# Performance work log

Hardware: AMD Instinct MI355X
Metric: run time of the kernel (lower is better)

## Reference

```python
import jax, jax.numpy as jnp
import numpy as np

N_NODES = 100000
N_EDGES = 1600000
HID = 128


def setup_inputs() -> dict:
    key = jax.random.key(0)
    ks = jax.random.split(key, 9)
    return {
        "x": jax.random.normal(ks[0], (N_NODES, 3), dtype=jnp.float32),
        "edge_index": jax.random.randint(ks[1], (2, N_EDGES), 0, N_NODES, dtype=jnp.int64),
        "W_lift": jax.random.normal(ks[2], (3, HID), dtype=jnp.float32) * 0.1,
        "b_lift": jax.random.normal(ks[3], (HID,), dtype=jnp.float32) * 0.1,
        "W_rel": jax.random.normal(ks[4], (HID, HID), dtype=jnp.float32) * 0.05,
        "b_rel": jax.random.normal(ks[5], (HID,), dtype=jnp.float32) * 0.05,
        "W_root": jax.random.normal(ks[6], (HID, HID), dtype=jnp.float32) * 0.05,
        "W_proj": jax.random.normal(ks[7], (HID, 1), dtype=jnp.float32) * 0.1,
        "b_proj": jax.random.normal(ks[8], (1,), dtype=jnp.float32) * 0.1,
    }


def reference(x, edge_index, W_lift, b_lift, W_rel, b_rel, W_root, W_proj, b_proj):
    # Lifting: [N, 3] -> [N, 128]
    h = x @ W_lift + b_lift
    # GraphConv (PyG): out_i = lin_rel(sum_{j in N(i)} h_j) + lin_root(h_i)
    src, dst = edge_index[0], edge_index[1]
    # gather neighbor features then scatter-add to targets
    agg = jax.ops.segment_sum(h[src], dst, num_segments=N_NODES)  # [N, 128]
    h = agg @ W_rel + b_rel + h @ W_root
    h = jnp.tanh(h)
    # Projection: [N, 128] -> [N, 1]
    return h @ W_proj + b_proj
```

## Files before the change

kernel.cpp:

```cpp
#include <hip/hip_runtime.h>
#include <stdint.h>

#define NN 100000
#define NE 1600000
#define HID 128

#define PSCALE 512.0f
#define PINV   (1.0f / 512.0f)
#define PBIAS  8.0f
#define FMASK  0x7FFFFULL

#define NBINS 391
#define NSLC  8
#define GCAP  768
#define NB3   391
#define TB3   512
#define EB    4096

__device__ __forceinline__ unsigned xcc_id() {
    unsigned x;
    asm volatile("s_getreg_b32 %0, hwreg(HW_REG_XCC_ID)" : "=s"(x));
    return x & (NSLC - 1);
}

__device__ __forceinline__ void prep_weights(
    const float* __restrict__ W_lift, const float* __restrict__ b_lift,
    const float* __restrict__ W_rel, const float* __restrict__ b_rel,
    const float* __restrict__ W_root, float* __restrict__ Wf) {
    int t = threadIdx.x;
    if (t >= HID) return;
    float lr0 = 0.f, lr1 = 0.f, lr2 = 0.f;
    float xr0 = 0.f, xr1 = 0.f, xr2 = 0.f;
    float blr = 0.f, bxr = 0.f;
    for (int k = 0; k < HID; ++k) {
        float wr = W_rel[k * HID + t];
        float wo = W_root[k * HID + t];
        float bl = b_lift[k];
        float a0 = W_lift[0 * HID + k];
        float a1 = W_lift[1 * HID + k];
        float a2 = W_lift[2 * HID + k];
        lr0 += a0 * wr; lr1 += a1 * wr; lr2 += a2 * wr;
        xr0 += a0 * wo; xr1 += a1 * wo; xr2 += a2 * wo;
        blr += bl * wr; bxr += bl * wo;
    }
    Wf[0 * HID + t] = lr0;
    Wf[1 * HID + t] = lr1;
    Wf[2 * HID + t] = lr2;
    Wf[3 * HID + t] = xr0;
    Wf[4 * HID + t] = xr1;
    Wf[5 * HID + t] = xr2;
    Wf[6 * HID + t] = blr;
    Wf[7 * HID + t] = b_rel[t] + bxr;
}

__global__ __launch_bounds__(TB3) void radix4_scatter_prep(
    const int* __restrict__ edges,
    unsigned* __restrict__ galloc,
    unsigned* __restrict__ records,
    const float* __restrict__ W_lift,
    const float* __restrict__ b_lift,
    const float* __restrict__ W_rel,
    const float* __restrict__ b_rel,
    const float* __restrict__ W_root,
    float* __restrict__ Wf) {
    if (blockIdx.x == NB3) {
        prep_weights(W_lift, b_lift, W_rel, b_rel, W_root, Wf);
        return;
    }
    __shared__ unsigned hist[NBINS];
    __shared__ unsigned base[NBINS];
    for (int j = threadIdx.x; j < NBINS; j += TB3) hist[j] = 0;
    __syncthreads();

    const unsigned myxcd = xcc_id();
    const int e0 = blockIdx.x * EB;
    int sreg[8], dreg[8];

#pragma unroll
    for (int k = 0; k < 2; ++k) {
        int eA = e0 + (k * TB3 + threadIdx.x) * 4;
        int4 sv, dv;
        if (eA + 3 < NE) {
            sv = *(const int4*)&edges[eA];
            dv = *(const int4*)&edges[NE + eA];
        } else {
            sv.x = (eA + 0 < NE) ? edges[eA + 0] : -1;
            sv.y = (eA + 1 < NE) ? edges[eA + 1] : -1;
            sv.z = (eA + 2 < NE) ? edges[eA + 2] : -1;
            sv.w = (eA + 3 < NE) ? edges[eA + 3] : -1;
            dv.x = (eA + 0 < NE) ? edges[NE + eA + 0] : -1;
            dv.y = (eA + 1 < NE) ? edges[NE + eA + 1] : -1;
            dv.z = (eA + 2 < NE) ? edges[NE + eA + 2] : -1;
            dv.w = (eA + 3 < NE) ? edges[NE + eA + 3] : -1;
        }
        int ss[4] = { sv.x, sv.y, sv.z, sv.w };
        int dd[4] = { dv.x, dv.y, dv.z, dv.w };
#pragma unroll
        for (int j = 0; j < 4; ++j) {
            bool ok = ((unsigned)ss[j] < NN) && ((unsigned)dd[j] < NN);
            sreg[k * 4 + j] = ok ? ss[j] : -1;
            dreg[k * 4 + j] = ok ? dd[j] : -1;
            if (ok) atomicAdd(&hist[dd[j] >> 8], 1u);
        }
    }
    __syncthreads();
    for (int j = threadIdx.x; j < NBINS; j += TB3) {
        unsigned c = hist[j];
        base[j] = c ? atomicAdd(&galloc[myxcd * NBINS + j], c) : 0u;
        hist[j] = 0;
    }
    __syncthreads();
#pragma unroll
    for (int i = 0; i < 8; ++i) {
        int d = dreg[i];
        if (d < 0) continue;
        int b = d >> 8;
        unsigned pos = base[b] + atomicAdd(&hist[b], 1u);
        if (pos < GCAP)
            records[((size_t)myxcd * NBINS + b) * GCAP + pos] =
                ((unsigned)sreg[i] << 8) | (unsigned)(d & 255);
    }
}

__global__ __launch_bounds__(256) void accum4_node_kernel(
    const unsigned* __restrict__ galloc,
    const unsigned* __restrict__ records,
    const float* __restrict__ x,
    const float* __restrict__ Wf,
    const float* __restrict__ W_proj,
    const float* __restrict__ b_proj,
    float* __restrict__ out) {
    __shared__ unsigned long long acc[256];
    __shared__ float sWt[HID][8];
    __shared__ float sP[HID];
    const int tid = threadIdx.x;
    const int b = blockIdx.x;

    acc[tid] = 0ULL;
    for (int j = tid; j < 8 * HID; j += 256) {
        int r = j >> 7;
        int t = j & (HID - 1);
        sWt[t][r] = Wf[j];
    }
    for (int j = tid; j < HID; j += 256) sP[j] = W_proj[j];
    __syncthreads();

#pragma unroll
    for (int sl = 0; sl < NSLC; ++sl) {
        unsigned cnt = galloc[sl * NBINS + b];
        if (cnt > GCAP) cnt = GCAP;
        const unsigned* rec = records + ((size_t)sl * NBINS + b) * GCAP;
        for (unsigned i = tid; i < cnt; i += 256) {
            unsigned r = rec[i];
            unsigned src = r >> 8;
            const float* xp = x + 3 * (size_t)src;
            unsigned long long u0 = min((unsigned)__float2int_rn((xp[0] + PBIAS) * PSCALE), 8191u);
            unsigned long long u1 = min((unsigned)__float2int_rn((xp[1] + PBIAS) * PSCALE), 8191u);
            unsigned long long u2 = min((unsigned)__float2int_rn((xp[2] + PBIAS) * PSCALE), 8191u);
            atomicAdd(&acc[r & 255u],
                      u0 | (u1 << 19) | (u2 << 38) | (1ULL << 57));
        }
    }
    __syncthreads();

    int node = b * 256 + tid;
    if (node >= NN) return;

    unsigned long long p = acc[tid];
    float degf = (float)(unsigned)(p >> 57);
    float a0 = (float)(unsigned)(p & FMASK) * PINV - PBIAS * degf;
    float a1 = (float)(unsigned)((p >> 19) & FMASK) * PINV - PBIAS * degf;
    float a2 = (float)(unsigned)((p >> 38) & FMASK) * PINV - PBIAS * degf;

    float x0 = x[3 * node + 0];
    float x1 = x[3 * node + 1];
    float x2 = x[3 * node + 2];

    float s = 0.f;
#pragma unroll 8
    for (int t = 0; t < HID; ++t) {
        float4 A = *(const float4*)&sWt[t][0];
        float4 B = *(const float4*)&sWt[t][4];
        float h = B.w
                + a0 * A.x + a1 * A.y + a2 * A.z
                + x0 * A.w + x1 * B.x + x2 * B.y
                + degf * B.z;
        float th = 1.f - 2.f / (__expf(2.f * h) + 1.f);
        s += th * sP[t];
    }
    out[node] = s + b_proj[0];
}

__global__ __launch_bounds__(256) void scatter_prep_kernel(
    const int* __restrict__ edges,
    const float* __restrict__ x,
    unsigned long long* __restrict__ aggp,
    const float* __restrict__ W_lift,
    const float* __restrict__ b_lift,
    const float* __restrict__ W_rel,
    const float* __restrict__ b_rel,
    const float* __restrict__ W_root,
    float* __restrict__ Wf) {
    if (blockIdx.x == 0) {
        prep_weights(W_lift, b_lift, W_rel, b_rel, W_root, Wf);
        return;
    }
    int e = (blockIdx.x - 1) * blockDim.x + threadIdx.x;
    if (e >= NE) return;
    int s = edges[e];
    int d = edges[NE + e];
    if ((unsigned)s >= NN || (unsigned)d >= NN) return;
    float x0 = x[3 * s + 0];
    float x1 = x[3 * s + 1];
    float x2 = x[3 * s + 2];
    unsigned long long u0 = (unsigned)__float2int_rn((x0 + PBIAS) * PSCALE);
    unsigned long long u1 = (unsigned)__float2int_rn((x1 + PBIAS) * PSCALE);
    unsigned long long u2 = (unsigned)__float2int_rn((x2 + PBIAS) * PSCALE);
    atomicAdd(&aggp[d], u0 | (u1 << 19) | (u2 << 38) | (1ULL << 57));
}

__global__ __launch_bounds__(256) void node_kernel(
    const float* __restrict__ x,
    const unsigned long long* __restrict__ aggp,
    const float* __restrict__ Wf,
    const float* __restrict__ W_proj,
    const float* __restrict__ b_proj,
    float* __restrict__ out) {
    __shared__ float sWt[HID][8];
    __shared__ float sP[HID];
    for (int j = threadIdx.x; j < 8 * HID; j += blockDim.x) {
        int r = j >> 7;
        int t = j & (HID - 1);
        sWt[t][r] = Wf[j];
    }
    for (int j = threadIdx.x; j < HID; j += blockDim.x) sP[j] = W_proj[j];
    __syncthreads();

    int i = blockIdx.x * blockDim.x + threadIdx.x;
    if (i >= NN) return;

    unsigned long long p = aggp[i];
    float degf = (float)(unsigned)(p >> 57);
    float a0 = (float)(unsigned)(p & FMASK) * PINV - PBIAS * degf;
    float a1 = (float)(unsigned)((p >> 19) & FMASK) * PINV - PBIAS * degf;
    float a2 = (float)(unsigned)((p >> 38) & FMASK) * PINV - PBIAS * degf;

    float x0 = x[3 * i + 0];
    float x1 = x[3 * i + 1];
    float x2 = x[3 * i + 2];

    float acc = 0.f;
#pragma unroll 8
    for (int t = 0; t < HID; ++t) {
        float4 A = *(const float4*)&sWt[t][0];
        float4 B = *(const float4*)&sWt[t][4];
        float h = B.w
                + a0 * A.x + a1 * A.y + a2 * A.z
                + x0 * A.w + x1 * B.x + x2 * B.y
                + degf * B.z;
        float th = 1.f - 2.f / (__expf(2.f * h) + 1.f);
        acc += th * sP[t];
    }
    out[i] = acc + b_proj[0];
}

extern "C" void kernel_launch(void* const* d_in, const int* in_sizes, int n_in,
                              void* d_out, int out_size, void* d_ws, size_t ws_size,
                              hipStream_t stream) {
    const float* x      = (const float*)d_in[0];
    const int*   edges  = (const int*)d_in[1];
    const float* W_lift = (const float*)d_in[2];
    const float* b_lift = (const float*)d_in[3];
    const float* W_rel  = (const float*)d_in[4];
    const float* b_rel  = (const float*)d_in[5];
    const float* W_root = (const float*)d_in[6];
    const float* W_proj = (const float*)d_in[7];
    const float* b_proj = (const float*)d_in[8];
    float* out = (float*)d_out;

    const size_t off_rec = 1 << 16;
    const size_t off_wf  = off_rec + (size_t)NSLC * NBINS * GCAP * 4;
    const size_t needed  = off_wf + 8 * HID * sizeof(float);

    if (ws_size >= needed) {
        unsigned* galloc = (unsigned*)d_ws;
        unsigned* records = (unsigned*)((char*)d_ws + off_rec);
        float* Wf = (float*)((char*)d_ws + off_wf);

        hipMemsetAsync(galloc, 0, NSLC * NBINS * sizeof(unsigned), stream);
        radix4_scatter_prep<<<NB3 + 1, TB3, 0, stream>>>(
            edges, galloc, records, W_lift, b_lift, W_rel, b_rel, W_root, Wf);
        accum4_node_kernel<<<NBINS, 256, 0, stream>>>(
            galloc, records, x, Wf, W_proj, b_proj, out);
    } else {
        unsigned long long* aggp = (unsigned long long*)d_ws;
        float* Wf = (float*)((char*)d_ws + (size_t)NN * 8);
        hipMemsetAsync(aggp, 0, (size_t)NN * 8, stream);
        scatter_prep_kernel<<<1 + (NE + 255) / 256, 256, 0, stream>>>(
            edges, x, aggp, W_lift, b_lift, W_rel, b_rel, W_root, Wf);
        node_kernel<<<(NN + 255) / 256, 256, 0, stream>>>(
            x, aggp, Wf, W_proj, b_proj, out);
    }
}
```

Measured before the change: 129.0 us.

## Widen accum kernel to 1024 threads, split slices and hidden dim across warps

The accumulation/node kernel now runs 1024 threads per block instead of 256. In the gather phase each group of 128 threads handles one XCD slice's records concurrently instead of looping over the eight slices. In the node phase the 128 hidden units are split into four groups of 32, and the partial sums are reduced through shared memory. With only 391 blocks on the GPU, this raises parallelism per block, at the cost of an extra barrier, a shared-memory reduction, and heavier LDS atomic contention.

```diff
diff --git a/kernel.cpp b/kernel.cpp
--- a/kernel.cpp
+++ b/kernel.cpp
@@ -16,6 +16,7 @@
 #define NB3   391
 #define TB3   512
 #define EB    4096
+#define TBA   1024
 
 __device__ __forceinline__ unsigned xcc_id() {
     unsigned x;
@@ -122,7 +123,7 @@
     }
 }
 
-__global__ __launch_bounds__(256) void accum4_node_kernel(
+__global__ __launch_bounds__(TBA) void accum4_node_kernel(
     const unsigned* __restrict__ galloc,
     const unsigned* __restrict__ records,
     const float* __restrict__ x,
@@ -133,24 +134,26 @@
     __shared__ unsigned long long acc[256];
     __shared__ float sWt[HID][8];
     __shared__ float sP[HID];
+    __shared__ float sPart[TBA];
     const int tid = threadIdx.x;
     const int b = blockIdx.x;
 
-    acc[tid] = 0ULL;
-    for (int j = tid; j < 8 * HID; j += 256) {
+    if (tid < 256) acc[tid] = 0ULL;
+    for (int j = tid; j < 8 * HID; j += TBA) {
         int r = j >> 7;
         int t = j & (HID - 1);
         sWt[t][r] = Wf[j];
     }
-    for (int j = tid; j < HID; j += 256) sP[j] = W_proj[j];
-    __syncthreads();
-
-#pragma unroll
-    for (int sl = 0; sl < NSLC; ++sl) {
+    for (int j = tid; j < HID; j += TBA) sP[j] = W_proj[j];
+    __syncthreads();
+
+    {
+        const int sl = tid >> 7;
+        const int l  = tid & 127;
         unsigned cnt = galloc[sl * NBINS + b];
         if (cnt > GCAP) cnt = GCAP;
         const unsigned* rec = records + ((size_t)sl * NBINS + b) * GCAP;
-        for (unsigned i = tid; i < cnt; i += 256) {
+        for (unsigned i = l; i < cnt; i += 128) {
             unsigned r = rec[i];
             unsigned src = r >> 8;
             const float* xp = x + 3 * (size_t)src;
@@ -163,32 +166,36 @@
     }
     __syncthreads();
 
-    int node = b * 256 + tid;
-    if (node >= NN) return;
-
-    unsigned long long p = acc[tid];
-    float degf = (float)(unsigned)(p >> 57);
-    float a0 = (float)(unsigned)(p & FMASK) * PINV - PBIAS * degf;
-    float a1 = (float)(unsigned)((p >> 19) & FMASK) * PINV - PBIAS * degf;
-    float a2 = (float)(unsigned)((p >> 38) & FMASK) * PINV - PBIAS * degf;
-
-    float x0 = x[3 * node + 0];
-    float x1 = x[3 * node + 1];
-    float x2 = x[3 * node + 2];
-
+    const int nl = tid & 255;
+    const int g  = tid >> 8;
+    int node = b * 256 + nl;
     float s = 0.f;
+    if (node < NN) {
+        unsigned long long p = acc[nl];
+        float degf = (float)(unsigned)(p >> 57);
+        float a0 = (float)(unsigned)(p & FMASK) * PINV - PBIAS * degf;
+        float a1 = (float)(unsigned)((p >> 19) & FMASK) * PINV - PBIAS * degf;
+        float a2 = (float)(unsigned)((p >> 38) & FMASK) * PINV - PBIAS * degf;
+        float x0 = x[3 * node + 0];
+        float x1 = x[3 * node + 1];
+        float x2 = x[3 * node + 2];
 #pragma unroll 8
-    for (int t = 0; t < HID; ++t) {
-        float4 A = *(const float4*)&sWt[t][0];
-        float4 B = *(const float4*)&sWt[t][4];
-        float h = B.w
-                + a0 * A.x + a1 * A.y + a2 * A.z
-                + x0 * A.w + x1 * B.x + x2 * B.y
-                + degf * B.z;
-        float th = 1.f - 2.f / (__expf(2.f * h) + 1.f);
-        s += th * sP[t];
-    }
-    out[node] = s + b_proj[0];
+        for (int t = g * 32; t < g * 32 + 32; ++t) {
+            float4 A = *(const float4*)&sWt[t][0];
+            float4 B = *(const float4*)&sWt[t][4];
+            float h = B.w
+                    + a0 * A.x + a1 * A.y + a2 * A.z
+                    + x0 * A.w + x1 * B.x + x2 * B.y
+                    + degf * B.z;
+            float th = 1.f - 2.f / (__expf(2.f * h) + 1.f);
+            s += th * sP[t];
+        }
+    }
+    sPart[tid] = s;
+    __syncthreads();
+    if (tid < 256 && node < NN)
+        out[node] = sPart[tid] + sPart[tid + 256] + sPart[tid + 512]
+                  + sPart[tid + 768] + b_proj[0];
 }
 
 __global__ __launch_bounds__(256) void scatter_prep_kernel(
@@ -290,7 +297,7 @@
         hipMemsetAsync(galloc, 0, NSLC * NBINS * sizeof(unsigned), stream);
         radix4_scatter_prep<<<NB3 + 1, TB3, 0, stream>>>(
             edges, galloc, records, W_lift, b_lift, W_rel, b_rel, W_root, Wf);
-        accum4_node_kernel<<<NBINS, 256, 0, stream>>>(
+        accum4_node_kernel<<<NBINS, TBA, 0, stream>>>(
             galloc, records, x, Wf, W_proj, b_proj, out);
     } else {
         unsigned long long* aggp = (unsigned long long*)d_ws;
```

Result: faster. 117.7 us (-8.8%).
